# Performance work log

Hardware: AMD Instinct MI355X
Metric: run time of the kernel (lower is better)

The kernel has to match this reference:

```python
import jax, jax.numpy as jnp
import numpy as np

B, I, O = 262144, 32, 32


def setup_inputs() -> dict:
    key = jax.random.key(0)
    k1, k2 = jax.random.split(key)
    # scalar-per-sample input, positive so sqrt arg is mostly valid
    x = jax.random.uniform(k1, (B,), dtype=jnp.float32)
    # xavier-uniform-like init, biased negative so (x - fd)/sigma^2 >= 0
    # for most elements (avoids the degenerate all-NaN fallback path)
    fuzzy_degree = -jnp.abs(jax.random.normal(k2, (I, O), dtype=jnp.float32)) * 0.1
    sigma = jnp.ones((I, O), dtype=jnp.float32)  # nn.init.ones_
    return {"x": x, "fuzzy_degree": fuzzy_degree, "sigma": sigma}


def reference(x, fuzzy_degree, sigma):
    # vectorized form of: for v in x: exp(-sum(sqrt((v - fd)/sigma**2)))
    # diff: [B, I, O] via broadcasting the scalar sample against [I, O] params
    diff = (x[:, None, None] - fuzzy_degree) / (sigma ** 2)
    s = jnp.sum(jnp.sqrt(diff), axis=(1, 2))  # [B]
    out = jnp.exp(-s)
    # original: if isnan(fuzzy_out_i) -> append the raw input sample
    return jnp.where(jnp.isnan(out), x, out)
```

## Files before the change

kernel.cpp:

```cpp
#include <hip/hip_runtime.h>


constexpr int NPAR  = 1024;
constexpr int BLOCK = 256;
constexpr float S0_CUTOFF = 104.0f;
constexpr float FIN_MAX   = 3.0e38f;

__global__ __launch_bounds__(BLOCK) void fuzzy_fused(
    const float* __restrict__ x,
    const float* __restrict__ fd,
    const float* __restrict__ sigma,
    float* __restrict__ out,
    int B)
{
    __shared__ float2 p[NPAR];
    __shared__ float  ssum[BLOCK];
    __shared__ int    sok[BLOCK];
    __shared__ int    block_slow;

    const int tid = threadIdx.x;

    float local = 0.0f;
    int ok = 1;
    for (int k = tid; k < NPAR; k += BLOCK) {
        float sg  = sigma[k];
        float inv = 1.0f / (sg * sg);
        float c   = -fd[k] * inv;
        p[k] = make_float2(inv, c);
        if (!(inv > 0.0f) || !(inv <= FIN_MAX) ||
            !(c >= 0.0f)  || !(c   <= FIN_MAX)) ok = 0;
        local += __builtin_amdgcn_sqrtf(c);
    }
    ssum[tid] = local;
    sok[tid]  = ok;
    if (tid == 0) block_slow = 0;
    __syncthreads();
    for (int s = BLOCK / 2; s > 0; s >>= 1) {
        if (tid < s) { ssum[tid] += ssum[tid + s]; sok[tid] &= sok[tid + s]; }
        __syncthreads();
    }
    const bool guard = sok[0] && (ssum[0] >= S0_CUTOFF);

    const int base = (blockIdx.x * BLOCK + tid) * 4;
    float4 xv = make_float4(0.0f, 0.0f, 0.0f, 0.0f);
    const bool full4 = (base + 3 < B);
    if (full4) {
        xv = *(const float4*)(x + base);
    } else if (base < B) {
        float* xs = (float*)&xv;
        for (int j = 0; j < 4 && base + j < B; ++j) xs[j] = x[base + j];
    }

    const bool lane_fast = guard &&
        (xv.x >= 0.0f) && (xv.y >= 0.0f) &&
        (xv.z >= 0.0f) && (xv.w >= 0.0f);
    if (!lane_fast) block_slow = 1;
    __syncthreads();

    if (!block_slow) {
        if (full4) {
            *(float4*)(out + base) = make_float4(0.0f, 0.0f, 0.0f, 0.0f);
        } else {
            for (int j = 0; j < 4 && base + j < B; ++j) out[base + j] = 0.0f;
        }
        return;
    }

    const float* xs = (const float*)&xv;
    float r[4];
    for (int j = 0; j < 4; ++j) {
        const float v = xs[j];
        float s0 = 0.0f, s1 = 0.0f, s2 = 0.0f, s3 = 0.0f;
#pragma unroll 2
        for (int k = 0; k < NPAR; k += 4) {
            float2 p0 = p[k + 0];
            float2 p1 = p[k + 1];
            float2 p2 = p[k + 2];
            float2 p3 = p[k + 3];
            s0 += __builtin_amdgcn_sqrtf(fmaf(v, p0.x, p0.y));
            s1 += __builtin_amdgcn_sqrtf(fmaf(v, p1.x, p1.y));
            s2 += __builtin_amdgcn_sqrtf(fmaf(v, p2.x, p2.y));
            s3 += __builtin_amdgcn_sqrtf(fmaf(v, p3.x, p3.y));
        }
        float s = (s0 + s1) + (s2 + s3);
        float o = __expf(-s);
        r[j] = (o != o) ? v : o;
    }
    if (full4) {
        *(float4*)(out + base) = make_float4(r[0], r[1], r[2], r[3]);
    } else {
        for (int j = 0; j < 4 && base + j < B; ++j) out[base + j] = r[j];
    }
}

extern "C" void kernel_launch(void* const* d_in, const int* in_sizes, int n_in,
                              void* d_out, int out_size, void* d_ws, size_t ws_size,
                              hipStream_t stream) {
    const float* x     = (const float*)d_in[0];
    const float* fd    = (const float*)d_in[1];
    const float* sigma = (const float*)d_in[2];
    float* out  = (float*)d_out;
    const int B = in_sizes[0];

    const int grid = (B + BLOCK * 4 - 1) / (BLOCK * 4);
    fuzzy_fused<<<grid, BLOCK, 0, stream>>>(x, fd, sigma, out, B);
}
```

Before: 59.10 us.

## Replace shared-memory tree reduction with wave shuffles and per-thread fast-path exit

```diff
diff --git a/kernel.cpp b/kernel.cpp
--- a/kernel.cpp
+++ b/kernel.cpp
@@ -3,8 +3,8 @@
 
 constexpr int NPAR  = 1024;
 constexpr int BLOCK = 256;
-constexpr float S0_CUTOFF = 104.0f;
-constexpr float FIN_MAX   = 3.0e38f;
+constexpr int VPT   = 4;
+constexpr float S0_CUTOFF = 128.0f;
 
 __global__ __launch_bounds__(BLOCK) void fuzzy_fused(
     const float* __restrict__ x,
@@ -13,83 +13,77 @@
     float* __restrict__ out,
     int B)
 {
-    __shared__ float2 p[NPAR];
-    __shared__ float  ssum[BLOCK];
-    __shared__ int    sok[BLOCK];
-    __shared__ int    block_slow;
-
-    const int tid = threadIdx.x;
+    __shared__ float wsum[BLOCK / 64];
+    __shared__ int   wok[BLOCK / 64];
+    const int tid  = threadIdx.x;
+    const int wave = tid >> 6;
 
     float local = 0.0f;
     int ok = 1;
-    for (int k = tid; k < NPAR; k += BLOCK) {
-        float sg  = sigma[k];
-        float inv = 1.0f / (sg * sg);
-        float c   = -fd[k] * inv;
-        p[k] = make_float2(inv, c);
-        if (!(inv > 0.0f) || !(inv <= FIN_MAX) ||
-            !(c >= 0.0f)  || !(c   <= FIN_MAX)) ok = 0;
-        local += __builtin_amdgcn_sqrtf(c);
+    {
+        const int k = tid * 4;
+        const float4 f = *(const float4*)(fd + k);
+        const float4 g = *(const float4*)(sigma + k);
+        const float* fe = (const float*)&f;
+        const float* ge = (const float*)&g;
+#pragma unroll
+        for (int j = 0; j < 4; ++j) {
+            const float s2 = ge[j] * ge[j];
+            if (!(fe[j] <= 0.0f) || !(fe[j] >= -1.0e37f) ||
+                !(s2 >= 1.0e-30f) || !(s2 <= 1.0e30f)) ok = 0;
+            local += __builtin_amdgcn_sqrtf((-fe[j]) * __builtin_amdgcn_rcpf(s2));
+        }
     }
-    ssum[tid] = local;
-    sok[tid]  = ok;
-    if (tid == 0) block_slow = 0;
+#pragma unroll
+    for (int off = 32; off > 0; off >>= 1)
+        local += __shfl_xor(local, off, 64);
+    ok = __all(ok);
+    if ((tid & 63) == 0) { wsum[wave] = local; wok[wave] = ok; }
     __syncthreads();
-    for (int s = BLOCK / 2; s > 0; s >>= 1) {
-        if (tid < s) { ssum[tid] += ssum[tid + s]; sok[tid] &= sok[tid + s]; }
-        __syncthreads();
-    }
-    const bool guard = sok[0] && (ssum[0] >= S0_CUTOFF);
+    float total = 0.0f; int allok = 1;
+#pragma unroll
+    for (int w = 0; w < BLOCK / 64; ++w) { total += wsum[w]; allok &= wok[w]; }
 
-    const int base = (blockIdx.x * BLOCK + tid) * 4;
+    const int base = (blockIdx.x * BLOCK + tid) * VPT;
+    if (base >= B) return;
     float4 xv = make_float4(0.0f, 0.0f, 0.0f, 0.0f);
-    const bool full4 = (base + 3 < B);
+    const bool full4 = (base + VPT <= B);
     if (full4) {
         xv = *(const float4*)(x + base);
-    } else if (base < B) {
+    } else {
         float* xs = (float*)&xv;
-        for (int j = 0; j < 4 && base + j < B; ++j) xs[j] = x[base + j];
+        for (int j = 0; j < VPT && base + j < B; ++j) xs[j] = x[base + j];
     }
 
-    const bool lane_fast = guard &&
+    const bool fast = allok && (total >= S0_CUTOFF) &&
         (xv.x >= 0.0f) && (xv.y >= 0.0f) &&
         (xv.z >= 0.0f) && (xv.w >= 0.0f);
-    if (!lane_fast) block_slow = 1;
-    __syncthreads();
-
-    if (!block_slow) {
+    if (fast) {
         if (full4) {
             *(float4*)(out + base) = make_float4(0.0f, 0.0f, 0.0f, 0.0f);
         } else {
-            for (int j = 0; j < 4 && base + j < B; ++j) out[base + j] = 0.0f;
+            for (int j = 0; j < VPT && base + j < B; ++j) out[base + j] = 0.0f;
         }
         return;
     }
 
     const float* xs = (const float*)&xv;
-    float r[4];
-    for (int j = 0; j < 4; ++j) {
+    float r[VPT];
+#pragma unroll
+    for (int j = 0; j < VPT; ++j) {
         const float v = xs[j];
-        float s0 = 0.0f, s1 = 0.0f, s2 = 0.0f, s3 = 0.0f;
-#pragma unroll 2
-        for (int k = 0; k < NPAR; k += 4) {
-            float2 p0 = p[k + 0];
-            float2 p1 = p[k + 1];
-            float2 p2 = p[k + 2];
-            float2 p3 = p[k + 3];
-            s0 += __builtin_amdgcn_sqrtf(fmaf(v, p0.x, p0.y));
-            s1 += __builtin_amdgcn_sqrtf(fmaf(v, p1.x, p1.y));
-            s2 += __builtin_amdgcn_sqrtf(fmaf(v, p2.x, p2.y));
-            s3 += __builtin_amdgcn_sqrtf(fmaf(v, p3.x, p3.y));
+        float s = 0.0f;
+        for (int k = 0; k < NPAR; ++k) {
+            const float sg = sigma[k];
+            s += __builtin_amdgcn_sqrtf((v - fd[k]) / (sg * sg));
         }
-        float s = (s0 + s1) + (s2 + s3);
-        float o = __expf(-s);
+        const float o = __expf(-s);
         r[j] = (o != o) ? v : o;
     }
     if (full4) {
         *(float4*)(out + base) = make_float4(r[0], r[1], r[2], r[3]);
     } else {
-        for (int j = 0; j < 4 && base + j < B; ++j) out[base + j] = r[j];
+        for (int j = 0; j < VPT && base + j < B; ++j) out[base + j] = r[j];
     }
 }
 
@@ -102,6 +96,6 @@
     float* out  = (float*)d_out;
     const int B = in_sizes[0];
 
-    const int grid = (B + BLOCK * 4 - 1) / (BLOCK * 4);
+    const int grid = (B + BLOCK * VPT - 1) / (BLOCK * VPT);
     fuzzy_fused<<<grid, BLOCK, 0, stream>>>(x, fd, sigma, out, B);
 }
```

After: 58.15 us. Within noise of the previous version (-1.6%).
